# Kernel optimization log

Hardware: AMD Instinct MI355X
Metric: run time of the kernel (lower is better)

The kernel has to match this reference:

```python
import jax, jax.numpy as jnp
import numpy as np

EPS = 1e-12


def setup_inputs() -> dict:
    key = jax.random.key(0)
    k1, k2 = jax.random.split(key)
    ide_feats = jax.random.normal(k1, (4096, 256), dtype=jnp.float32)
    u_feats = jax.random.normal(k2, (16384, 256), dtype=jnp.float32)
    return {"ide_feats": ide_feats, "u_feats": u_feats}


def reference(ide_feats, u_feats):
    # euclidean_dist: sqrt(sum((x_i - y_j)^2) + eps) -> [N, M]
    # computed via the GEMM expansion to avoid the [N, M, D] intermediate
    x2 = jnp.sum(ide_feats * ide_feats, axis=-1)[:, None]   # [N, 1]
    y2 = jnp.sum(u_feats * u_feats, axis=-1)[None, :]       # [1, M]
    xy = jnp.einsum('nd,md->nm', ide_feats, u_feats)        # [N, M]
    d2 = jnp.maximum(x2 + y2 - 2.0 * xy, 0.0)
    dists = jnp.sqrt(d2 + EPS)                              # [N, M]
    d = jnp.mean(dists, axis=-1)                            # [N]
    # dist_loss: sum_{i,j} sqrt((d_i - d_j)^2 + eps)
    diff = d[:, None] - d[None, :]                          # [N, N]
    loss = jnp.sum(jnp.sqrt(diff * diff + EPS))
    return loss
```

## Files before the change

### kernel.cpp

```cpp
#include <hip/hip_runtime.h>
#include <hip/hip_bf16.h>
#include <cstdint>

#define N_IDE 4096
#define M_U   16384
#define D_DIM 256
#define EPSF  1e-12f
#define INV_M (1.0f / 16384.0f)

typedef _Float16 f16x8 __attribute__((ext_vector_type(8)));
typedef float    f32x4 __attribute__((ext_vector_type(4)));

__device__ __forceinline__ void gll16(const void* g, void* l) {
  __builtin_amdgcn_global_load_lds(
      (const __attribute__((address_space(1))) void*)(uintptr_t)g,
      (__attribute__((address_space(3))) void*)(uint32_t)(uintptr_t)l,
      16, 0, 0);
}

__device__ __forceinline__ unsigned short f2h_bits(float f) {
  _Float16 h = (_Float16)f;
  return __builtin_bit_cast(unsigned short, h);
}

__global__ __launch_bounds__(256) void k_conv(const float* __restrict__ ide,
                                              const float* __restrict__ u,
                                              unsigned short* __restrict__ Ah,
                                              unsigned short* __restrict__ Bh,
                                              float* __restrict__ x2,
                                              float* __restrict__ y2) {
  int gw = (blockIdx.x * 256 + threadIdx.x) >> 6;
  int l  = threadIdx.x & 63;
  const float4* src;
  ushort4* dst;
  float* nrm;
  if (gw < N_IDE) {
    src = (const float4*)(ide + (size_t)gw * D_DIM);
    dst = (ushort4*)(Ah + (size_t)gw * D_DIM);
    nrm = x2 + gw;
  } else {
    int r = gw - N_IDE;
    src = (const float4*)(u + (size_t)r * D_DIM);
    dst = (ushort4*)(Bh + (size_t)r * D_DIM);
    nrm = y2 + r;
  }
  float4 v = src[l];
  float s = v.x * v.x + v.y * v.y + v.z * v.z + v.w * v.w;
  ushort4 o;
  o.x = f2h_bits(v.x); o.y = f2h_bits(v.y);
  o.z = f2h_bits(v.z); o.w = f2h_bits(v.w);
  dst[l] = o;
#pragma unroll
  for (int m = 1; m <= 32; m <<= 1) s += __shfl_xor(s, m, 64);
  if (l == 0) *nrm = s;
}

__global__ __launch_bounds__(512, 2) void k_gemm(const unsigned short* __restrict__ Ah,
                                                 const unsigned short* __restrict__ Bh,
                                                 const float* __restrict__ x2,
                                                 const float* __restrict__ y2,
                                                 float* __restrict__ partial) {
  __shared__ __align__(16) unsigned short sA[128 * 256];
  __shared__ float rowacc[8][128];

  const int t    = threadIdx.x;
  const int w    = t >> 6;
  const int l    = t & 63;
  const int lrow = l & 15;
  const int lhi  = l >> 4;
  const int bx   = blockIdx.x;
  const int by   = blockIdx.y;

#pragma unroll
  for (int i = 0; i < 8; ++i) {
    int L = i * 512 + t;
    int row = L >> 5;
    int p = L & 31;
    int c = (p & 24) | ((p & 7) ^ (row & 7));
    gll16(Ah + (size_t)(by * 128 + row) * D_DIM + c * 8,
          sA + (size_t)(i * 512 + w * 64) * 8);
  }
  __syncthreads();

  const int colbase = bx * 512 + w * 64;

  const unsigned short* bptr[4];
#pragma unroll
  for (int nj = 0; nj < 4; ++nj)
    bptr[nj] = Bh + (size_t)(colbase + nj * 16 + lrow) * D_DIM + lhi * 8;

  f32x4 acc[8][4];
#pragma unroll
  for (int mi = 0; mi < 8; ++mi)
#pragma unroll
    for (int nj = 0; nj < 4; ++nj)
      acc[mi][nj] = (f32x4){0.f, 0.f, 0.f, 0.f};

  f16x8 bfb[2][4];
#pragma unroll
  for (int nj = 0; nj < 4; ++nj) bfb[0][nj] = *(const f16x8*)(bptr[nj]);

#pragma unroll
  for (int kt = 0; kt < 8; ++kt) {
    if (kt < 7) {
#pragma unroll
      for (int nj = 0; nj < 4; ++nj)
        bfb[(kt + 1) & 1][nj] = *(const f16x8*)(bptr[nj] + (kt + 1) * 32);
    }
    const int lc = kt * 4 + lhi;
    const int pc = (lc & 24) | ((lc & 7) ^ (lrow & 7));
    f16x8 af[8];
#pragma unroll
    for (int mi = 0; mi < 8; ++mi)
      af[mi] = *(const f16x8*)(sA + (size_t)(mi * 16 + lrow) * 256 + pc * 8);
#pragma unroll
    for (int mi = 0; mi < 8; ++mi)
#pragma unroll
      for (int nj = 0; nj < 4; ++nj)
        acc[mi][nj] = __builtin_amdgcn_mfma_f32_16x16x32_f16(af[mi], bfb[kt & 1][nj],
                                                             acc[mi][nj], 0, 0, 0);
  }

  float yv[4];
#pragma unroll
  for (int nj = 0; nj < 4; ++nj) yv[nj] = y2[colbase + nj * 16 + lrow];

#pragma unroll
  for (int mi = 0; mi < 8; ++mi) {
    float4 x2v = *(const float4*)&x2[by * 128 + mi * 16 + lhi * 4];
    float xr[4] = {x2v.x, x2v.y, x2v.z, x2v.w};
    float rv[4];
#pragma unroll
    for (int rr = 0; rr < 4; ++rr) {
      float ssum = 0.f;
#pragma unroll
      for (int nj = 0; nj < 4; ++nj) {
        float d2 = xr[rr] + yv[nj] - 2.0f * acc[mi][nj][rr];
        d2 = fmaxf(d2, 0.0f);
        ssum += __builtin_amdgcn_sqrtf(d2 + EPSF);
      }
      ssum += __shfl_xor(ssum, 1, 64);
      ssum += __shfl_xor(ssum, 2, 64);
      ssum += __shfl_xor(ssum, 4, 64);
      ssum += __shfl_xor(ssum, 8, 64);
      rv[rr] = ssum;
    }
    if (lrow == 0)
      *(float4*)&rowacc[w][mi * 16 + lhi * 4] = make_float4(rv[0], rv[1], rv[2], rv[3]);
  }

  __syncthreads();
  if (t < 128) {
    float s = 0.f;
#pragma unroll
    for (int ww = 0; ww < 8; ++ww) s += rowacc[ww][t];
    partial[(size_t)bx * N_IDE + by * 128 + t] = s;
  }
}

__global__ __launch_bounds__(256) void k_dsum(const float* __restrict__ partial,
                                              float* __restrict__ d) {
  int k = blockIdx.x * 256 + threadIdx.x;
  float s = 0.f;
#pragma unroll
  for (int b = 0; b < 32; ++b) s += partial[(size_t)b * N_IDE + k];
  d[k] = s;
}

__global__ __launch_bounds__(256) void k_loss(const float* __restrict__ d,
                                              float* __restrict__ out) {
  __shared__ float sd[N_IDE];
  __shared__ float wsum[4];
  int t = threadIdx.x;
  for (int k = t; k < N_IDE; k += 256) sd[k] = d[k];
  __syncthreads();
  int tid = blockIdx.x * 256 + t;
  int i   = tid >> 4;
  int jl  = tid & 15;
  float di = sd[i];
  float s  = 0.f;
  for (int k = 0; k < 256; ++k) {
    float diff = (di - sd[jl + k * 16]) * INV_M;
    s += __builtin_amdgcn_sqrtf(diff * diff + EPSF);
  }
#pragma unroll
  for (int m = 1; m <= 32; m <<= 1) s += __shfl_xor(s, m, 64);
  if ((t & 63) == 0) wsum[t >> 6] = s;
  __syncthreads();
  if (t == 0) atomicAdd(out, wsum[0] + wsum[1] + wsum[2] + wsum[3]);
}

extern "C" void kernel_launch(void* const* d_in, const int* in_sizes, int n_in,
                              void* d_out, int out_size, void* d_ws, size_t ws_size,
                              hipStream_t stream) {
  (void)in_sizes; (void)n_in; (void)out_size; (void)ws_size;
  const float* ide = (const float*)d_in[0];
  const float* u   = (const float*)d_in[1];
  float* out = (float*)d_out;

  char* ws = (char*)d_ws;
  size_t off = 0;
  unsigned short* Ah = (unsigned short*)(ws + off); off += (size_t)N_IDE * D_DIM * 2;
  unsigned short* Bh = (unsigned short*)(ws + off); off += (size_t)M_U  * D_DIM * 2;
  float* x2      = (float*)(ws + off); off += (size_t)N_IDE * 4;
  float* y2      = (float*)(ws + off); off += (size_t)M_U * 4;
  float* partial = (float*)(ws + off); off += (size_t)32 * N_IDE * 4;
  float* dvec    = (float*)(ws + off); off += (size_t)N_IDE * 4;

  hipMemsetAsync(d_out, 0, sizeof(float), stream);
  k_conv<<<(N_IDE + M_U) / 4, 256, 0, stream>>>(ide, u, Ah, Bh, x2, y2);
  k_gemm<<<dim3(32, 32), 512, 0, stream>>>(Ah, Bh, x2, y2, partial);
  k_dsum<<<N_IDE / 256, 256, 0, stream>>>(partial, dvec);
  k_loss<<<256, 256, 0, stream>>>(dvec, out);
}
```

Before: 141.2 us.

## Restructure distance GEMM with LDS double-buffered A/B tiles and fewer launches

The GEMM kernel now uses 256 threads in a 2x2 wave layout. It stages both A and B k-slices through double-buffered, swizzled LDS and iterates over four 128-column chunks per block, instead of keeping a full 128x256 A tile and streaming B from global memory into registers. The separate dsum kernel and the memset are removed: partial row sums are stored transposed and reduced inside k_loss, and out is zeroed in k_conv. The aim is to improve B reuse and occupancy and to cut launch overhead, at the cost of more barriers per k-step and a smaller per-wave tile.

```diff
diff --git a/kernel.cpp b/kernel.cpp
--- a/kernel.cpp
+++ b/kernel.cpp
@@ -28,7 +28,9 @@
                                               unsigned short* __restrict__ Ah,
                                               unsigned short* __restrict__ Bh,
                                               float* __restrict__ x2,
-                                              float* __restrict__ y2) {
+                                              float* __restrict__ y2,
+                                              float* __restrict__ out) {
+  if (blockIdx.x == 0 && threadIdx.x == 0) out[0] = 0.f;
   int gw = (blockIdx.x * 256 + threadIdx.x) >> 6;
   int l  = threadIdx.x & 63;
   const float4* src;
@@ -55,124 +57,128 @@
   if (l == 0) *nrm = s;
 }
 
-__global__ __launch_bounds__(512, 2) void k_gemm(const unsigned short* __restrict__ Ah,
+__global__ __launch_bounds__(256, 3) void k_gemm(const unsigned short* __restrict__ Ah,
                                                  const unsigned short* __restrict__ Bh,
                                                  const float* __restrict__ x2,
                                                  const float* __restrict__ y2,
                                                  float* __restrict__ partial) {
-  __shared__ __align__(16) unsigned short sA[128 * 256];
-  __shared__ float rowacc[8][128];
+  __shared__ __align__(16) unsigned short sA[2][4096];
+  __shared__ __align__(16) unsigned short sB[2][4096];
+  __shared__ float rowacc[2][128];
 
   const int t    = threadIdx.x;
   const int w    = t >> 6;
   const int l    = t & 63;
   const int lrow = l & 15;
   const int lhi  = l >> 4;
+  const int wm   = w >> 1, wn = w & 1;
   const int bx   = blockIdx.x;
   const int by   = blockIdx.y;
 
-#pragma unroll
-  for (int i = 0; i < 8; ++i) {
-    int L = i * 512 + t;
-    int row = L >> 5;
-    int p = L & 31;
-    int c = (p & 24) | ((p & 7) ^ (row & 7));
-    gll16(Ah + (size_t)(by * 128 + row) * D_DIM + c * 8,
-          sA + (size_t)(i * 512 + w * 64) * 8);
-  }
+  rowacc[t >> 7][t & 127] = 0.f;
+
+  const int r0  = t >> 2;
+  const int kc0 = (t & 3) ^ ((r0 >> 1) & 3);
+  const size_t soff = (size_t)r0 * D_DIM + kc0 * 8;
+
+  const unsigned short* Ab = Ah + (size_t)(by * 128) * D_DIM;
+
+  const int sl = (lhi ^ ((lrow >> 1) & 3)) * 8;
+
+  for (int cr = 0; cr < 4; ++cr) {
+    const unsigned short* Bb = Bh + (size_t)(bx * 512 + cr * 128) * D_DIM;
+
+    auto stg = [&](int kt, int buf) {
+      const unsigned short* sa = Ab + kt * 32 + soff;
+      unsigned short* da = &sA[buf][w * 512];
+      gll16(sa, da);
+      gll16(sa + (size_t)64 * D_DIM, da + 2048);
+      const unsigned short* sb = Bb + kt * 32 + soff;
+      unsigned short* db = &sB[buf][w * 512];
+      gll16(sb, db);
+      gll16(sb + (size_t)64 * D_DIM, db + 2048);
+    };
+
+    f32x4 acc[4][4];
+#pragma unroll
+    for (int mi = 0; mi < 4; ++mi)
+#pragma unroll
+      for (int nj = 0; nj < 4; ++nj)
+        acc[mi][nj] = (f32x4){0.f, 0.f, 0.f, 0.f};
+
+    stg(0, 0);
+    __syncthreads();
+
+    for (int kt = 0; kt < 8; ++kt) {
+      if (kt < 7) stg(kt + 1, (kt + 1) & 1);
+
+      const unsigned short* pa = &sA[kt & 1][0];
+      const unsigned short* pb = &sB[kt & 1][0];
+      f16x8 af[4], bf[4];
+#pragma unroll
+      for (int mi = 0; mi < 4; ++mi)
+        af[mi] = *(const f16x8*)(pa + (wm * 64 + mi * 16 + lrow) * 32 + sl);
+#pragma unroll
+      for (int nj = 0; nj < 4; ++nj)
+        bf[nj] = *(const f16x8*)(pb + (wn * 64 + nj * 16 + lrow) * 32 + sl);
+
+#pragma unroll
+      for (int mi = 0; mi < 4; ++mi)
+#pragma unroll
+        for (int nj = 0; nj < 4; ++nj)
+          acc[mi][nj] = __builtin_amdgcn_mfma_f32_16x16x32_f16(af[mi], bf[nj],
+                                                               acc[mi][nj], 0, 0, 0);
+      __syncthreads();
+    }
+
+    float yv[4];
+#pragma unroll
+    for (int nj = 0; nj < 4; ++nj)
+      yv[nj] = y2[bx * 512 + cr * 128 + wn * 64 + nj * 16 + lrow];
+
+#pragma unroll
+    for (int mi = 0; mi < 4; ++mi) {
+      float4 x2v = *(const float4*)&x2[by * 128 + wm * 64 + mi * 16 + lhi * 4];
+      float xr[4] = {x2v.x, x2v.y, x2v.z, x2v.w};
+#pragma unroll
+      for (int rr = 0; rr < 4; ++rr) {
+        float ssum = 0.f;
+#pragma unroll
+        for (int nj = 0; nj < 4; ++nj) {
+          float d2 = xr[rr] + yv[nj] - 2.0f * acc[mi][nj][rr];
+          d2 = fmaxf(d2, 0.0f);
+          ssum += __builtin_amdgcn_sqrtf(d2 + EPSF);
+        }
+        ssum += __shfl_xor(ssum, 1, 64);
+        ssum += __shfl_xor(ssum, 2, 64);
+        ssum += __shfl_xor(ssum, 4, 64);
+        ssum += __shfl_xor(ssum, 8, 64);
+        if (lrow == 0)
+          rowacc[wn][wm * 64 + mi * 16 + lhi * 4 + rr] += ssum;
+      }
+    }
+  }
+
   __syncthreads();
-
-  const int colbase = bx * 512 + w * 64;
-
-  const unsigned short* bptr[4];
-#pragma unroll
-  for (int nj = 0; nj < 4; ++nj)
-    bptr[nj] = Bh + (size_t)(colbase + nj * 16 + lrow) * D_DIM + lhi * 8;
-
-  f32x4 acc[8][4];
-#pragma unroll
-  for (int mi = 0; mi < 8; ++mi)
-#pragma unroll
-    for (int nj = 0; nj < 4; ++nj)
-      acc[mi][nj] = (f32x4){0.f, 0.f, 0.f, 0.f};
-
-  f16x8 bfb[2][4];
-#pragma unroll
-  for (int nj = 0; nj < 4; ++nj) bfb[0][nj] = *(const f16x8*)(bptr[nj]);
-
-#pragma unroll
-  for (int kt = 0; kt < 8; ++kt) {
-    if (kt < 7) {
-#pragma unroll
-      for (int nj = 0; nj < 4; ++nj)
-        bfb[(kt + 1) & 1][nj] = *(const f16x8*)(bptr[nj] + (kt + 1) * 32);
-    }
-    const int lc = kt * 4 + lhi;
-    const int pc = (lc & 24) | ((lc & 7) ^ (lrow & 7));
-    f16x8 af[8];
-#pragma unroll
-    for (int mi = 0; mi < 8; ++mi)
-      af[mi] = *(const f16x8*)(sA + (size_t)(mi * 16 + lrow) * 256 + pc * 8);
-#pragma unroll
-    for (int mi = 0; mi < 8; ++mi)
-#pragma unroll
-      for (int nj = 0; nj < 4; ++nj)
-        acc[mi][nj] = __builtin_amdgcn_mfma_f32_16x16x32_f16(af[mi], bfb[kt & 1][nj],
-                                                             acc[mi][nj], 0, 0, 0);
-  }
-
-  float yv[4];
-#pragma unroll
-  for (int nj = 0; nj < 4; ++nj) yv[nj] = y2[colbase + nj * 16 + lrow];
-
-#pragma unroll
-  for (int mi = 0; mi < 8; ++mi) {
-    float4 x2v = *(const float4*)&x2[by * 128 + mi * 16 + lhi * 4];
-    float xr[4] = {x2v.x, x2v.y, x2v.z, x2v.w};
-    float rv[4];
-#pragma unroll
-    for (int rr = 0; rr < 4; ++rr) {
-      float ssum = 0.f;
-#pragma unroll
-      for (int nj = 0; nj < 4; ++nj) {
-        float d2 = xr[rr] + yv[nj] - 2.0f * acc[mi][nj][rr];
-        d2 = fmaxf(d2, 0.0f);
-        ssum += __builtin_amdgcn_sqrtf(d2 + EPSF);
-      }
-      ssum += __shfl_xor(ssum, 1, 64);
-      ssum += __shfl_xor(ssum, 2, 64);
-      ssum += __shfl_xor(ssum, 4, 64);
-      ssum += __shfl_xor(ssum, 8, 64);
-      rv[rr] = ssum;
-    }
-    if (lrow == 0)
-      *(float4*)&rowacc[w][mi * 16 + lhi * 4] = make_float4(rv[0], rv[1], rv[2], rv[3]);
-  }
-
-  __syncthreads();
-  if (t < 128) {
-    float s = 0.f;
-#pragma unroll
-    for (int ww = 0; ww < 8; ++ww) s += rowacc[ww][t];
-    partial[(size_t)bx * N_IDE + by * 128 + t] = s;
-  }
-}
-
-__global__ __launch_bounds__(256) void k_dsum(const float* __restrict__ partial,
-                                              float* __restrict__ d) {
-  int k = blockIdx.x * 256 + threadIdx.x;
-  float s = 0.f;
-#pragma unroll
-  for (int b = 0; b < 32; ++b) s += partial[(size_t)b * N_IDE + k];
-  d[k] = s;
-}
-
-__global__ __launch_bounds__(256) void k_loss(const float* __restrict__ d,
+  if (t < 128)
+    partial[(size_t)(by * 128 + t) * 32 + bx] = rowacc[0][t] + rowacc[1][t];
+}
+
+__global__ __launch_bounds__(256) void k_loss(const float* __restrict__ partial,
                                               float* __restrict__ out) {
   __shared__ float sd[N_IDE];
   __shared__ float wsum[4];
   int t = threadIdx.x;
-  for (int k = t; k < N_IDE; k += 256) sd[k] = d[k];
+  for (int k = t; k < N_IDE; k += 256) {
+    const float4* p = (const float4*)(partial + (size_t)k * 32);
+    float4 a = p[0];
+#pragma unroll
+    for (int b = 1; b < 8; ++b) {
+      float4 q = p[b];
+      a.x += q.x; a.y += q.y; a.z += q.z; a.w += q.w;
+    }
+    sd[k] = (a.x + a.y) + (a.z + a.w);
+  }
   __syncthreads();
   int tid = blockIdx.x * 256 + t;
   int i   = tid >> 4;
@@ -204,12 +210,9 @@
   unsigned short* Bh = (unsigned short*)(ws + off); off += (size_t)M_U  * D_DIM * 2;
   float* x2      = (float*)(ws + off); off += (size_t)N_IDE * 4;
   float* y2      = (float*)(ws + off); off += (size_t)M_U * 4;
-  float* partial = (float*)(ws + off); off += (size_t)32 * N_IDE * 4;
-  float* dvec    = (float*)(ws + off); off += (size_t)N_IDE * 4;
-
-  hipMemsetAsync(d_out, 0, sizeof(float), stream);
-  k_conv<<<(N_IDE + M_U) / 4, 256, 0, stream>>>(ide, u, Ah, Bh, x2, y2);
-  k_gemm<<<dim3(32, 32), 512, 0, stream>>>(Ah, Bh, x2, y2, partial);
-  k_dsum<<<N_IDE / 256, 256, 0, stream>>>(partial, dvec);
-  k_loss<<<256, 256, 0, stream>>>(dvec, out);
-}
+  float* partial = (float*)(ws + off); off += (size_t)N_IDE * 32 * 4;
+
+  k_conv<<<(N_IDE + M_U) / 4, 256, 0, stream>>>(ide, u, Ah, Bh, x2, y2, out);
+  k_gemm<<<dim3(32, 32), 256, 0, stream>>>(Ah, Bh, x2, y2, partial);
+  k_loss<<<256, 256, 0, stream>>>(partial, out);
+}
```

Measured after the change: 161.7 us. 1.15x slower.
